# Optimization experiments

Hardware: AMD Instinct MI355X
Metric: run time of the kernel (lower is better)

## Reference

```python
import jax, jax.numpy as jnp
import numpy as np

N_NODES = 50000
N_EDGES = 800000
D_IN = 128
D_HID = 128
D_OUT = 128


def setup_inputs() -> dict:
    key = jax.random.key(0)
    ks = jax.random.split(key, 5)
    x = jax.random.normal(ks[0], (N_NODES, D_IN), dtype=jnp.float32)
    edge_index = jax.random.randint(ks[1], (2, N_EDGES), 0, N_NODES, dtype=jnp.int64)
    # Glorot-ish init for the two GCN linear weights (PyG uses glorot)
    W1 = jax.random.normal(ks[2], (D_IN, D_HID), dtype=jnp.float32) * (1.0 / np.sqrt(D_IN))
    b1 = jnp.zeros((D_HID,), dtype=jnp.float32)
    W2 = jax.random.normal(ks[3], (D_HID, D_OUT), dtype=jnp.float32) * (1.0 / np.sqrt(D_HID))
    b2 = jnp.zeros((D_OUT,), dtype=jnp.float32)
    return {"x": x, "edge_index": edge_index, "W1": W1, "b1": b1, "W2": W2, "b2": b2}


def _gcn_layer(x, W, b, src, dst, dinv):
    """PyG GCNConv: h = xW; out[j] = sum_{(i->j)} dinv[i]*dinv[j]*h[i] + dinv[j]^2*h[j] (self-loop) + b."""
    n = x.shape[0]
    h = x @ W                                   # [N, D_out]
    coef = (dinv[src] * dinv[dst])[:, None]     # [E, 1] symmetric norm
    msg = h[src] * coef                         # [E, D_out] gather + scale
    agg = jax.ops.segment_sum(msg, dst, num_segments=n)  # scatter-add
    agg = agg + h * (dinv * dinv)[:, None]      # self-loop contribution
    return agg + b


def reference(x, edge_index, W1, b1, W2, b2):
    src = edge_index[0]
    dst = edge_index[1]
    n = x.shape[0]
    # degree over target nodes, including the added self-loop (+1)
    deg = jax.ops.segment_sum(jnp.ones_like(dst, dtype=x.dtype), dst, num_segments=n) + 1.0
    dinv = jax.lax.rsqrt(deg)
    h = jax.nn.relu(_gcn_layer(x, W1, b1, src, dst, dinv))
    return _gcn_layer(h, W2, b2, src, dst, dinv)
```

## Files before the change

### kernel.cpp

```cpp
#include <hip/hip_runtime.h>
#include <hip/hip_fp16.h>

#define NN 50000
#define NE 800000
#define D 128
#define NBLK ((NN + 255) / 256)

typedef __attribute__((ext_vector_type(8))) short bf16x8;
typedef __attribute__((ext_vector_type(4))) float f32x4;

static __device__ __forceinline__ unsigned short f2bf(float f) {
    unsigned u = __builtin_bit_cast(unsigned, f);
    unsigned r = (u + 0x7fffu + ((u >> 16) & 1u)) >> 16;
    return (unsigned short)r;
}
static __device__ __forceinline__ float bf2f(unsigned short h) {
    unsigned u = ((unsigned)h) << 16;
    return __builtin_bit_cast(float, u);
}

__global__ __launch_bounds__(256) void k_zero_cnt(int* __restrict__ cnt) {
    int i = blockIdx.x * 256 + threadIdx.x;
    if (i < NN) cnt[i] = 0;
}

__global__ __launch_bounds__(256) void k_count(const int* __restrict__ dst, int* __restrict__ cnt) {
    int e = blockIdx.x * 256 + threadIdx.x;
    if (e < NE) atomicAdd(&cnt[dst[e]], 1);
}

__global__ __launch_bounds__(256) void k_scan_partial(const int* __restrict__ cnt, int* __restrict__ blockSums) {
    __shared__ int s[256];
    int t = threadIdx.x;
    int i = blockIdx.x * 256 + t;
    s[t] = (i < NN) ? cnt[i] : 0;
    __syncthreads();
    for (int off = 128; off > 0; off >>= 1) {
        if (t < off) s[t] += s[t + off];
        __syncthreads();
    }
    if (t == 0) blockSums[blockIdx.x] = s[0];
}

__global__ __launch_bounds__(256) void k_scan_blocks(int* __restrict__ blockSums, int* __restrict__ row_ptr,
                                                     int2* __restrict__ csr) {
    __shared__ int s[256];
    int t = threadIdx.x;
    int v = (t < NBLK) ? blockSums[t] : 0;
    s[t] = v;
    __syncthreads();
    for (int off = 1; off < 256; off <<= 1) {
        int y = (t >= off) ? s[t - off] : 0;
        __syncthreads();
        s[t] += y;
        __syncthreads();
    }
    if (t < NBLK) blockSums[t] = s[t] - v;
    if (t == 0) row_ptr[NN] = NE;
    if (t < 8) csr[NE + t] = make_int2(0, 0);
}

__global__ __launch_bounds__(256) void k_scan_final(const int* __restrict__ cnt, const int* __restrict__ blockOffs,
                                                    int* __restrict__ row_ptr, int* __restrict__ cursor,
                                                    float* __restrict__ dinv) {
    __shared__ int s[256];
    int t = threadIdx.x;
    int i = blockIdx.x * 256 + t;
    int v = (i < NN) ? cnt[i] : 0;
    s[t] = v;
    __syncthreads();
    for (int off = 1; off < 256; off <<= 1) {
        int y = (t >= off) ? s[t - off] : 0;
        __syncthreads();
        s[t] += y;
        __syncthreads();
    }
    if (i < NN) {
        int excl = s[t] - v + blockOffs[blockIdx.x];
        row_ptr[i] = excl;
        cursor[i] = excl;
        dinv[i] = rsqrtf((float)v + 1.0f);
    }
}

__global__ __launch_bounds__(256) void k_fill(const int* __restrict__ src, const int* __restrict__ dst,
                                              const float* __restrict__ dinv, int* __restrict__ cursor,
                                              int2* __restrict__ csr) {
    int e = blockIdx.x * 256 + threadIdx.x;
    if (e < NE) {
        int sN = src[e], dN = dst[e];
        int pos = atomicAdd(&cursor[dN], 1);
        float c = dinv[sN] * dinv[dN];
        csr[pos] = make_int2(sN, __float_as_int(c));
    }
}

__global__ __launch_bounds__(256) void k_prepw(const float* __restrict__ W1, const float* __restrict__ W2,
                                               char* __restrict__ img1, char* __restrict__ img2) {
    int b = blockIdx.x;
    const float* W = (b < 64) ? W1 : W2;
    char* img = (b < 64) ? img1 : img2;
    int e = (b & 63) * 256 + threadIdx.x;
    int k = e >> 7, n = e & 127;
    float f = W[e];
    unsigned short hi = f2bf(f);
    float rem = f - bf2f(hi);
    unsigned short lo = f2bf(rem);
    unsigned off = (unsigned)((n << 8) + (k << 1)) ^ (unsigned)((n & 7) << 4);
    *(unsigned short*)(img + off) = hi;
    *(unsigned short*)(img + 32768 + off) = lo;
}

template <bool RELU_IN>
__global__ __launch_bounds__(256) void k_mgemm(const float* __restrict__ A, const char* __restrict__ wimg,
                                               __half* __restrict__ H) {
    __shared__ char lds[65536];
    const int t = threadIdx.x;

    {
        const float4* gv = (const float4*)wimg;
        float4* lv = (float4*)lds;
#pragma unroll
        for (int i = 0; i < 16; ++i) lv[i * 256 + t] = gv[i * 256 + t];
    }
    __syncthreads();

    const int lane = t & 63;
    const int wv = t >> 6;
    const int r0 = blockIdx.x * 64 + wv * 16;
    const int rl = lane & 15;
    const int g = lane >> 4;
    int arow = r0 + rl;
    if (arow >= NN) arow = NN - 1;
    const float* ar = A + (size_t)arow * D + g * 8;

    f32x4 acc[8];
#pragma unroll
    for (int j = 0; j < 8; ++j) acc[j] = (f32x4){0.f, 0.f, 0.f, 0.f};

#pragma unroll
    for (int ks = 0; ks < 4; ++ks) {
        float av[8];
        float4 p0 = *(const float4*)(ar + ks * 32);
        float4 p1 = *(const float4*)(ar + ks * 32 + 4);
        av[0] = p0.x; av[1] = p0.y; av[2] = p0.z; av[3] = p0.w;
        av[4] = p1.x; av[5] = p1.y; av[6] = p1.z; av[7] = p1.w;
        bf16x8 ah, al;
#pragma unroll
        for (int i = 0; i < 8; ++i) {
            float a = RELU_IN ? fmaxf(av[i], 0.f) : av[i];
            unsigned short h = f2bf(a);
            ah[i] = (short)h;
            al[i] = (short)f2bf(a - bf2f(h));
        }
        const int kofs = (ks * 32 + g * 8) << 1;
#pragma unroll
        for (int j = 0; j < 8; ++j) {
            int n = j * 16 + rl;
            unsigned off = (unsigned)((n << 8) + kofs) ^ (unsigned)((n & 7) << 4);
            bf16x8 bh = *(const bf16x8*)(lds + off);
            bf16x8 bl = *(const bf16x8*)(lds + 32768 + off);
            acc[j] = __builtin_amdgcn_mfma_f32_16x16x32_bf16(ah, bh, acc[j], 0, 0, 0);
            acc[j] = __builtin_amdgcn_mfma_f32_16x16x32_bf16(ah, bl, acc[j], 0, 0, 0);
            acc[j] = __builtin_amdgcn_mfma_f32_16x16x32_bf16(al, bh, acc[j], 0, 0, 0);
        }
    }

#pragma unroll
    for (int j = 0; j < 8; ++j) {
#pragma unroll
        for (int i = 0; i < 4; ++i) {
            int row = r0 + g * 4 + i;
            if (row < NN) H[(size_t)row * D + j * 16 + rl] = __float2half(acc[j][i]);
        }
    }
}

__global__ __launch_bounds__(256) void k_pull(const __half2* __restrict__ H2, const float* __restrict__ dinv,
                                              const float* __restrict__ b, const int* __restrict__ row_ptr,
                                              const int2* __restrict__ csr, float* __restrict__ out) {
    int wid = (blockIdx.x * 256 + threadIdx.x) >> 6;
    int lane = threadIdx.x & 63;
    int node = __builtin_amdgcn_readfirstlane(wid);

    float di = dinv[node];
    float s2 = di * di;
    float2 self = __half22float2(H2[(size_t)node * 64 + lane]);
    float2 bb = ((const float2*)b)[lane];
    float2 a0, a1;
    a0.x = fmaf(self.x, s2, bb.x);
    a0.y = fmaf(self.y, s2, bb.y);
    a1.x = a1.y = 0.f;

    int beg = row_ptr[node];
    int end = row_ptr[node + 1];
    for (int i = beg; i < end; i += 4) {
        int2 e0 = csr[i];
        int2 e1 = csr[i + 1];
        int2 e2 = csr[i + 2];
        int2 e3 = csr[i + 3];
        float c0 = __int_as_float(e0.y);
        float c1 = (i + 1 < end) ? __int_as_float(e1.y) : 0.f;
        float c2 = (i + 2 < end) ? __int_as_float(e2.y) : 0.f;
        float c3 = (i + 3 < end) ? __int_as_float(e3.y) : 0.f;
        float2 v0 = __half22float2(H2[(size_t)e0.x * 64 + lane]);
        float2 v1 = __half22float2(H2[(size_t)e1.x * 64 + lane]);
        float2 v2 = __half22float2(H2[(size_t)e2.x * 64 + lane]);
        float2 v3 = __half22float2(H2[(size_t)e3.x * 64 + lane]);
        a0.x = fmaf(v0.x, c0, a0.x); a0.y = fmaf(v0.y, c0, a0.y);
        a1.x = fmaf(v1.x, c1, a1.x); a1.y = fmaf(v1.y, c1, a1.y);
        a0.x = fmaf(v2.x, c2, a0.x); a0.y = fmaf(v2.y, c2, a0.y);
        a1.x = fmaf(v3.x, c3, a1.x); a1.y = fmaf(v3.y, c3, a1.y);
    }
    float2 r;
    r.x = a0.x + a1.x;
    r.y = a0.y + a1.y;
    ((float2*)out)[(size_t)node * 64 + lane] = r;
}

extern "C" void kernel_launch(void* const* d_in, const int* in_sizes, int n_in,
                              void* d_out, int out_size, void* d_ws, size_t ws_size,
                              hipStream_t stream) {
    const float* x  = (const float*)d_in[0];
    const int*   ei = (const int*)d_in[1];
    const float* W1 = (const float*)d_in[2];
    const float* b1 = (const float*)d_in[3];
    const float* W2 = (const float*)d_in[4];
    const float* b2 = (const float*)d_in[5];
    float* out = (float*)d_out;

    const int* src = ei;
    const int* dst = ei + NE;

    char* ws = (char*)d_ws;
    int*    cnt       = (int*)   (ws + 0);
    int*    row_ptr   = (int*)   (ws + 204800);
    int*    cursor    = (int*)   (ws + 409600);
    int*    blockSums = (int*)   (ws + 614400);
    float*  dinv      = (float*) (ws + 615424);
    char*   wimg1     = (char*)  (ws + 819200);
    char*   wimg2     = (char*)  (ws + 884736);
    int2*   csr       = (int2*)  (ws + 950272);
    __half* h         = (__half*)(ws + 7350400);
    __half2* h2       = (__half2*)h;

    const int nBlkEdge = (NE + 255) / 256;
    const int nBlkGemm = (NN + 63) / 64;
    const int nBlkPull = NN / 4;

    k_zero_cnt<<<NBLK, 256, 0, stream>>>(cnt);
    k_count<<<nBlkEdge, 256, 0, stream>>>(dst, cnt);
    k_scan_partial<<<NBLK, 256, 0, stream>>>(cnt, blockSums);
    k_scan_blocks<<<1, 256, 0, stream>>>(blockSums, row_ptr, csr);
    k_scan_final<<<NBLK, 256, 0, stream>>>(cnt, blockSums, row_ptr, cursor, dinv);
    k_fill<<<nBlkEdge, 256, 0, stream>>>(src, dst, dinv, cursor, csr);
    k_prepw<<<128, 256, 0, stream>>>(W1, W2, wimg1, wimg2);

    k_mgemm<false><<<nBlkGemm, 256, 0, stream>>>(x, wimg1, h);
    k_pull<<<nBlkPull, 256, 0, stream>>>(h2, dinv, b1, row_ptr, csr, out);

    k_mgemm<true><<<nBlkGemm, 256, 0, stream>>>(out, wimg2, h);
    k_pull<<<nBlkPull, 256, 0, stream>>>(h2, dinv, b2, row_ptr, csr, out);
}
```

Before: 255.4 us.

## Compress CSR to 16-bit sources and split pull edges across lane groups

The CSR entries shrink from an int2 (source index plus precomputed coefficient) to a 16-bit source index. The normalisation coefficient is now recomputed in the pull kernel from dinv, and the fill kernel no longer gathers dinv. The pull kernel is restructured so that each group of 16 lanes handles a different edge, with 16-byte vector loads of fp16 rows and a shuffle reduction across groups at the end. The aim is to cut CSR traffic and per-edge instruction overhead, at the cost of an extra random dinv gather per edge and a dependence on the node count fitting in 16 bits.

```diff
diff --git a/kernel.cpp b/kernel.cpp
--- a/kernel.cpp
+++ b/kernel.cpp
@@ -42,8 +42,7 @@
     if (t == 0) blockSums[blockIdx.x] = s[0];
 }
 
-__global__ __launch_bounds__(256) void k_scan_blocks(int* __restrict__ blockSums, int* __restrict__ row_ptr,
-                                                     int2* __restrict__ csr) {
+__global__ __launch_bounds__(256) void k_scan_blocks(int* __restrict__ blockSums, int* __restrict__ row_ptr) {
     __shared__ int s[256];
     int t = threadIdx.x;
     int v = (t < NBLK) ? blockSums[t] : 0;
@@ -57,7 +56,6 @@
     }
     if (t < NBLK) blockSums[t] = s[t] - v;
     if (t == 0) row_ptr[NN] = NE;
-    if (t < 8) csr[NE + t] = make_int2(0, 0);
 }
 
 __global__ __launch_bounds__(256) void k_scan_final(const int* __restrict__ cnt, const int* __restrict__ blockOffs,
@@ -84,14 +82,11 @@
 }
 
 __global__ __launch_bounds__(256) void k_fill(const int* __restrict__ src, const int* __restrict__ dst,
-                                              const float* __restrict__ dinv, int* __restrict__ cursor,
-                                              int2* __restrict__ csr) {
+                                              int* __restrict__ cursor, unsigned short* __restrict__ csr) {
     int e = blockIdx.x * 256 + threadIdx.x;
     if (e < NE) {
-        int sN = src[e], dN = dst[e];
-        int pos = atomicAdd(&cursor[dN], 1);
-        float c = dinv[sN] * dinv[dN];
-        csr[pos] = make_int2(sN, __float_as_int(c));
+        int pos = atomicAdd(&cursor[dst[e]], 1);
+        csr[pos] = (unsigned short)src[e];
     }
 }
 
@@ -176,46 +171,66 @@
     }
 }
 
-__global__ __launch_bounds__(256) void k_pull(const __half2* __restrict__ H2, const float* __restrict__ dinv,
+__global__ __launch_bounds__(256) void k_pull(const __half* __restrict__ H, const float* __restrict__ dinv,
                                               const float* __restrict__ b, const int* __restrict__ row_ptr,
-                                              const int2* __restrict__ csr, float* __restrict__ out) {
+                                              const unsigned short* __restrict__ csr, float* __restrict__ out) {
     int wid = (blockIdx.x * 256 + threadIdx.x) >> 6;
     int lane = threadIdx.x & 63;
     int node = __builtin_amdgcn_readfirstlane(wid);
-
-    float di = dinv[node];
-    float s2 = di * di;
-    float2 self = __half22float2(H2[(size_t)node * 64 + lane]);
-    float2 bb = ((const float2*)b)[lane];
-    float2 a0, a1;
-    a0.x = fmaf(self.x, s2, bb.x);
-    a0.y = fmaf(self.y, s2, bb.y);
-    a1.x = a1.y = 0.f;
+    int rl = lane & 15;
+    int g = lane >> 4;
+
+    float dd = dinv[node];
+
+    float2 a0 = {0.f, 0.f}, a1 = {0.f, 0.f}, a2 = {0.f, 0.f}, a3 = {0.f, 0.f};
 
     int beg = row_ptr[node];
     int end = row_ptr[node + 1];
-    for (int i = beg; i < end; i += 4) {
-        int2 e0 = csr[i];
-        int2 e1 = csr[i + 1];
-        int2 e2 = csr[i + 2];
-        int2 e3 = csr[i + 3];
-        float c0 = __int_as_float(e0.y);
-        float c1 = (i + 1 < end) ? __int_as_float(e1.y) : 0.f;
-        float c2 = (i + 2 < end) ? __int_as_float(e2.y) : 0.f;
-        float c3 = (i + 3 < end) ? __int_as_float(e3.y) : 0.f;
-        float2 v0 = __half22float2(H2[(size_t)e0.x * 64 + lane]);
-        float2 v1 = __half22float2(H2[(size_t)e1.x * 64 + lane]);
-        float2 v2 = __half22float2(H2[(size_t)e2.x * 64 + lane]);
-        float2 v3 = __half22float2(H2[(size_t)e3.x * 64 + lane]);
-        a0.x = fmaf(v0.x, c0, a0.x); a0.y = fmaf(v0.y, c0, a0.y);
-        a1.x = fmaf(v1.x, c1, a1.x); a1.y = fmaf(v1.y, c1, a1.y);
-        a0.x = fmaf(v2.x, c2, a0.x); a0.y = fmaf(v2.y, c2, a0.y);
-        a1.x = fmaf(v3.x, c3, a1.x); a1.y = fmaf(v3.y, c3, a1.y);
-    }
-    float2 r;
-    r.x = a0.x + a1.x;
-    r.y = a0.y + a1.y;
-    ((float2*)out)[(size_t)node * 64 + lane] = r;
+    for (int i = beg + g; i < end; i += 4) {
+        int s = csr[i];
+        float c = dinv[s] * dd;
+        float4 raw = *(const float4*)(H + (size_t)s * D + rl * 8);
+        const __half2* hh = (const __half2*)&raw;
+        float2 f0 = __half22float2(hh[0]);
+        float2 f1 = __half22float2(hh[1]);
+        float2 f2 = __half22float2(hh[2]);
+        float2 f3 = __half22float2(hh[3]);
+        a0.x = fmaf(f0.x, c, a0.x); a0.y = fmaf(f0.y, c, a0.y);
+        a1.x = fmaf(f1.x, c, a1.x); a1.y = fmaf(f1.y, c, a1.y);
+        a2.x = fmaf(f2.x, c, a2.x); a2.y = fmaf(f2.y, c, a2.y);
+        a3.x = fmaf(f3.x, c, a3.x); a3.y = fmaf(f3.y, c, a3.y);
+    }
+
+    float v[8] = {a0.x, a0.y, a1.x, a1.y, a2.x, a2.y, a3.x, a3.y};
+#pragma unroll
+    for (int i = 0; i < 8; ++i) {
+        v[i] += __shfl_xor(v[i], 16);
+        v[i] += __shfl_xor(v[i], 32);
+    }
+
+    if (g == 0) {
+        float s2 = dd * dd;
+        float4 raw = *(const float4*)(H + (size_t)node * D + rl * 8);
+        const __half2* hh = (const __half2*)&raw;
+        float2 s0 = __half22float2(hh[0]);
+        float2 s1 = __half22float2(hh[1]);
+        float2 s2v = __half22float2(hh[2]);
+        float2 s3 = __half22float2(hh[3]);
+        float4 b0 = ((const float4*)b)[rl * 2];
+        float4 b1 = ((const float4*)b)[rl * 2 + 1];
+        float4 r0, r1;
+        r0.x = fmaf(s0.x, s2, v[0] + b0.x);
+        r0.y = fmaf(s0.y, s2, v[1] + b0.y);
+        r0.z = fmaf(s1.x, s2, v[2] + b0.z);
+        r0.w = fmaf(s1.y, s2, v[3] + b0.w);
+        r1.x = fmaf(s2v.x, s2, v[4] + b1.x);
+        r1.y = fmaf(s2v.y, s2, v[5] + b1.y);
+        r1.z = fmaf(s3.x, s2, v[6] + b1.z);
+        r1.w = fmaf(s3.y, s2, v[7] + b1.w);
+        float4* op = (float4*)(out + (size_t)node * D + rl * 8);
+        op[0] = r0;
+        op[1] = r1;
+    }
 }
 
 extern "C" void kernel_launch(void* const* d_in, const int* in_sizes, int n_in,
@@ -240,9 +255,8 @@
     float*  dinv      = (float*) (ws + 615424);
     char*   wimg1     = (char*)  (ws + 819200);
     char*   wimg2     = (char*)  (ws + 884736);
-    int2*   csr       = (int2*)  (ws + 950272);
-    __half* h         = (__half*)(ws + 7350400);
-    __half2* h2       = (__half2*)h;
+    unsigned short* csr = (unsigned short*)(ws + 950272);
+    __half* h         = (__half*)(ws + 2550784);
 
     const int nBlkEdge = (NE + 255) / 256;
     const int nBlkGemm = (NN + 63) / 64;
@@ -251,14 +265,14 @@
     k_zero_cnt<<<NBLK, 256, 0, stream>>>(cnt);
     k_count<<<nBlkEdge, 256, 0, stream>>>(dst, cnt);
     k_scan_partial<<<NBLK, 256, 0, stream>>>(cnt, blockSums);
-    k_scan_blocks<<<1, 256, 0, stream>>>(blockSums, row_ptr, csr);
+    k_scan_blocks<<<1, 256, 0, stream>>>(blockSums, row_ptr);
     k_scan_final<<<NBLK, 256, 0, stream>>>(cnt, blockSums, row_ptr, cursor, dinv);
-    k_fill<<<nBlkEdge, 256, 0, stream>>>(src, dst, dinv, cursor, csr);
+    k_fill<<<nBlkEdge, 256, 0, stream>>>(src, dst, cursor, csr);
     k_prepw<<<128, 256, 0, stream>>>(W1, W2, wimg1, wimg2);
 
     k_mgemm<false><<<nBlkGemm, 256, 0, stream>>>(x, wimg1, h);
-    k_pull<<<nBlkPull, 256, 0, stream>>>(h2, dinv, b1, row_ptr, csr, out);
+    k_pull<<<nBlkPull, 256, 0, stream>>>(h, dinv, b1, row_ptr, csr, out);
 
     k_mgemm<true><<<nBlkGemm, 256, 0, stream>>>(out, wimg2, h);
-    k_pull<<<nBlkPull, 256, 0, stream>>>(h2, dinv, b2, row_ptr, csr, out);
-}
+    k_pull<<<nBlkPull, 256, 0, stream>>>(h, dinv, b2, row_ptr, csr, out);
+}
```

Result: slower. 267.2 us (+4.6%).
